# Kernel tuning notes

Measured on AMD Instinct MI355X. Metric: run time of the kernel, lower is better.

## Reference

```python
import jax, jax.numpy as jnp
import numpy as np

N, E, D, H, OUT = 100000, 1600000, 64, 64, 4


def _glorot(key, i, o):
    s = (6.0 / (i + o)) ** 0.5
    return jax.random.uniform(key, (i, o), jnp.float32, -s, s)


def setup_inputs() -> dict:
    key = jax.random.key(0)
    ks = jax.random.split(key, 5)
    x = jax.random.normal(ks[0], (N, D), jnp.float32)
    edge_index = jax.random.randint(ks[1], (2, E), 0, N, jnp.int32)
    return {
        "x": x,
        "edge_index": edge_index,
        "W0": _glorot(ks[2], D, H), "b0": jnp.zeros((H,), jnp.float32),
        "W1": _glorot(ks[3], H, H), "b1": jnp.zeros((H,), jnp.float32),
        "W2": _glorot(ks[4], H, OUT), "b2": jnp.zeros((OUT,), jnp.float32),
    }


def _gcn_layer(x, src, dst, W, b):
    # WeightedGCNConv.forward: remove_self_loops, then gcn_norm with
    # add_self_loops=True (self-loop weight 1), symmetric normalization,
    # scatter-add aggregation, then Linear.
    n = x.shape[0]
    w = (src != dst).astype(x.dtype)           # zero out original self loops
    deg = jax.ops.segment_sum(w, dst, num_segments=n) + 1.0  # +1 from added self loop
    dis = jax.lax.rsqrt(deg)                   # deg >= 1, no inf
    norm = dis[src] * w * dis[dst]             # [E]
    agg = jax.ops.segment_sum(norm[:, None] * x[src], dst, num_segments=n)
    agg = agg + (dis * dis)[:, None] * x       # self-loop contribution
    return agg @ W + b


def reference(x, edge_index, W0, b0, W1, b1, W2, b2):
    src, dst = edge_index[0], edge_index[1]    # flow source_to_target
    # Dropout is identity in eval mode.
    h = jax.nn.relu(_gcn_layer(x, src, dst, W0, b0))
    h = jax.nn.relu(_gcn_layer(h, src, dst, W1, b1))
    return _gcn_layer(h, src, dst, W2, b2)     # [N, 4]
```

## Files before the change

### kernel.cpp

```cpp
#include <hip/hip_runtime.h>
#include <hip/hip_fp16.h>


#define BLK 256
#define NBITS 7
#define NBW   (1 << NBITS)
#define G     8
#define CHUNK 4096
#define EPT   (CHUNK / BLK)
#define CAPG  384
#define PAD   16

__global__ void k_binA(const int* __restrict__ src, const int* __restrict__ dst,
                       int* __restrict__ bcur, int* __restrict__ binned,
                       int E, int nb) {
    __shared__ int lcnt[1024];
    __shared__ int lbase[1024];
    int t = threadIdx.x;
    int g = blockIdx.x & (G - 1);
    for (int i = t; i < nb; i += BLK) lcnt[i] = 0;
    __syncthreads();

    int e0 = blockIdx.x * CHUNK;
    int bs[EPT], vs[EPT];
#pragma unroll
    for (int i = 0; i < EPT; ++i) {
        int e = e0 + i * BLK + t;
        bs[i] = -1;
        if (e < E) {
            int s = src[e], d = dst[e];
            if (s != d) {
                bs[i] = d >> NBITS;
                vs[i] = (s << NBITS) | (d & (NBW - 1));
                atomicAdd(&lcnt[bs[i]], 1);
            }
        }
    }
    __syncthreads();
    for (int i = t; i < nb; i += BLK) {
        int c = lcnt[i];
        lbase[i] = c ? atomicAdd(&bcur[(g * nb + i) * PAD], c) : 0;
    }
    __syncthreads();
    for (int i = t; i < nb; i += BLK) lcnt[i] = 0;
    __syncthreads();
#pragma unroll
    for (int i = 0; i < EPT; ++i) {
        if (bs[i] >= 0) {
            int p = lbase[bs[i]] + atomicAdd(&lcnt[bs[i]], 1);
            if (p < CAPG) binned[(size_t)(g * nb + bs[i]) * CAPG + p] = vs[i];
        }
    }
}

__global__ void k_bscan(const int* __restrict__ bcur, int* __restrict__ bbase, int nb) {
    __shared__ int sh[1024];
    int t = threadIdx.x;
    int v = 0;
    if (t < nb)
        for (int g = 0; g < G; ++g) v += min(bcur[(g * nb + t) * PAD], CAPG);
    sh[t] = v;
    __syncthreads();
    for (int off = 1; off < 1024; off <<= 1) {
        int u = (t >= off) ? sh[t - off] : 0;
        __syncthreads();
        sh[t] += u;
        __syncthreads();
    }
    if (t < nb) bbase[t] = sh[t] - v;
}

__global__ void k_binB(const int* __restrict__ bcur, const int* __restrict__ binned,
                       const int* __restrict__ bbase, int* __restrict__ rowstart,
                       float* __restrict__ dis, int* __restrict__ srcs,
                       int n, int nb) {
    __shared__ int cnt[NBW];
    __shared__ int scan[NBW];
    int b = blockIdx.x;
    int t = threadIdx.x;
    if (t < NBW) cnt[t] = 0;
    __syncthreads();
    for (int g = 0; g < G; ++g) {
        int m = min(bcur[(g * nb + b) * PAD], CAPG);
        const int* reg = binned + (size_t)(g * nb + b) * CAPG;
        for (int i = t; i < m; i += BLK)
            atomicAdd(&cnt[reg[i] & (NBW - 1)], 1);
    }
    __syncthreads();
    int c = 0;
    if (t < NBW) { c = cnt[t]; scan[t] = c; }
    __syncthreads();
    for (int off = 1; off < NBW; off <<= 1) {
        int u = (t < NBW && t >= off) ? scan[t - off] : 0;
        __syncthreads();
        if (t < NBW) scan[t] += u;
        __syncthreads();
    }
    int base = bbase[b];
    if (t < NBW) {
        int excl = scan[t] - c;
        int node = b * NBW + t;
        if (node < n) {
            rowstart[node] = base + excl;
            dis[node] = rsqrtf((float)c + 1.0f);
        }
        if (node == n) rowstart[n] = base + excl;
    }
    __syncthreads();
    if (t < NBW) scan[t] = scan[t] - c;
    __syncthreads();
    for (int g = 0; g < G; ++g) {
        int m = min(bcur[(g * nb + b) * PAD], CAPG);
        const int* reg = binned + (size_t)(g * nb + b) * CAPG;
        for (int i = t; i < m; i += BLK) {
            int v = reg[i];
            int p = atomicAdd(&scan[v & (NBW - 1)], 1);
            srcs[base + p] = v >> NBITS;
        }
    }
}

__global__ void k_gemm64(const float* __restrict__ in, const float* __restrict__ W,
                         const float* __restrict__ dis, __half* __restrict__ z16, int n) {
    __shared__ float rows[4][64];
    int c  = threadIdx.x & 63;
    int r4 = threadIdx.x >> 6;
    float Wr[64];
#pragma unroll
    for (int k = 0; k < 64; ++k) Wr[k] = W[k * 64 + c];
    const float4* rp = reinterpret_cast<const float4*>(&rows[r4][0]);
    for (long base = (long)blockIdx.x * 4; base < n; base += (long)gridDim.x * 4) {
        long row = base + r4;
        __syncthreads();
        if (row < n) rows[r4][c] = in[row * 64 + c];
        __syncthreads();
        if (row < n) {
            float acc = 0.0f;
#pragma unroll
            for (int k4 = 0; k4 < 16; ++k4) {
                float4 rv = rp[k4];
                acc = fmaf(rv.x, Wr[4 * k4 + 0], acc);
                acc = fmaf(rv.y, Wr[4 * k4 + 1], acc);
                acc = fmaf(rv.z, Wr[4 * k4 + 2], acc);
                acc = fmaf(rv.w, Wr[4 * k4 + 3], acc);
            }
            z16[row * 64 + c] = __float2half(dis[row] * acc);
        }
    }
}

__device__ __forceinline__ float4 gather_row(const float2* __restrict__ zrow,
                                             const int* __restrict__ rowstart,
                                             const int* __restrict__ srcs,
                                             int node, int lane, int p, int hi) {
    float4 acc = make_float4(0.f, 0.f, 0.f, 0.f);
    if (hi == 0) {
        float2 r = zrow[(long)node * 16 + p];
        float2 a = __half22float2(*reinterpret_cast<__half2*>(&r.x));
        float2 bq = __half22float2(*reinterpret_cast<__half2*>(&r.y));
        acc = make_float4(a.x, a.y, bq.x, bq.y);
    }
    int beg = rowstart[node], end = rowstart[node + 1];
    for (int base = beg; base < end; base += 64) {
        int m = min(end - base, 64);
        int s = (lane < m) ? srcs[base + lane] : 0;
        int mf = m & ~3;
#pragma unroll 8
        for (int j = 0; j < mf; j += 4) {
            int sj = __shfl(s, j + hi);
            float2 r = zrow[(long)sj * 16 + p];
            float2 a = __half22float2(*reinterpret_cast<__half2*>(&r.x));
            float2 bq = __half22float2(*reinterpret_cast<__half2*>(&r.y));
            acc.x += a.x; acc.y += a.y; acc.z += bq.x; acc.w += bq.y;
        }
        if (m & 3) {
            int idx = mf + hi;
            int sj = __shfl(s, idx < 64 ? idx : 63);
            if (idx < m) {
                float2 r = zrow[(long)sj * 16 + p];
                float2 a = __half22float2(*reinterpret_cast<__half2*>(&r.x));
                float2 bq = __half22float2(*reinterpret_cast<__half2*>(&r.y));
                acc.x += a.x; acc.y += a.y; acc.z += bq.x; acc.w += bq.y;
            }
        }
    }
    acc.x += __shfl_xor(acc.x, 16); acc.y += __shfl_xor(acc.y, 16);
    acc.z += __shfl_xor(acc.z, 16); acc.w += __shfl_xor(acc.w, 16);
    acc.x += __shfl_xor(acc.x, 32); acc.y += __shfl_xor(acc.y, 32);
    acc.z += __shfl_xor(acc.z, 32); acc.w += __shfl_xor(acc.w, 32);
    return acc;
}

__global__ void k_aggW1(const float2* __restrict__ zrow, const int* __restrict__ rowstart,
                        const int* __restrict__ srcs, const float* __restrict__ dis,
                        const float* __restrict__ b0, const float* __restrict__ W1,
                        __half* __restrict__ z1, int n) {
    __shared__ float hrow[4][64];
    int lane = threadIdx.x & 63;
    int wv   = threadIdx.x >> 6;
    int node = blockIdx.x * (BLK / 64) + wv;
    if (node >= n) return;
    int p = lane & 15, hi = lane >> 4;

    float4 acc = gather_row(zrow, rowstart, srcs, node, lane, p, hi);

    float dd = dis[node];
    float4 bb = reinterpret_cast<const float4*>(b0)[p];
    if (hi == 0) {
        float4 h;
        h.x = fmaxf(dd * acc.x + bb.x, 0.f);
        h.y = fmaxf(dd * acc.y + bb.y, 0.f);
        h.z = fmaxf(dd * acc.z + bb.z, 0.f);
        h.w = fmaxf(dd * acc.w + bb.w, 0.f);
        *reinterpret_cast<float4*>(&hrow[wv][4 * p]) = h;
    }
    asm volatile("s_waitcnt lgkmcnt(0)" ::: "memory");

    float Wr[64];
#pragma unroll
    for (int k = 0; k < 64; ++k) Wr[k] = W1[k * 64 + lane];
    const float4* hq = reinterpret_cast<const float4*>(&hrow[wv][0]);
    float o = 0.f;
#pragma unroll
    for (int k4 = 0; k4 < 16; ++k4) {
        float4 hv = hq[k4];
        o = fmaf(hv.x, Wr[4 * k4 + 0], o);
        o = fmaf(hv.y, Wr[4 * k4 + 1], o);
        o = fmaf(hv.z, Wr[4 * k4 + 2], o);
        o = fmaf(hv.w, Wr[4 * k4 + 3], o);
    }
    z1[(long)node * 64 + lane] = __float2half(dd * o);
}

__global__ void k_aggW2(const float2* __restrict__ zrow, const int* __restrict__ rowstart,
                        const int* __restrict__ srcs, const float* __restrict__ dis,
                        const float* __restrict__ b1, const float* __restrict__ W2,
                        float* __restrict__ y2, int n) {
    __shared__ float W2l[64 * 4];
    if (threadIdx.x < 256) W2l[threadIdx.x] = W2[threadIdx.x];
    __syncthreads();
    int lane = threadIdx.x & 63;
    int node = blockIdx.x * (BLK / 64) + (threadIdx.x >> 6);
    if (node >= n) return;
    int p = lane & 15, hi = lane >> 4;

    float4 acc = gather_row(zrow, rowstart, srcs, node, lane, p, hi);

    float dd = dis[node];
    float4 bb = reinterpret_cast<const float4*>(b1)[p];
    float h0 = fmaxf(dd * acc.x + bb.x, 0.f);
    float h1 = fmaxf(dd * acc.y + bb.y, 0.f);
    float h2 = fmaxf(dd * acc.z + bb.z, 0.f);
    float h3 = fmaxf(dd * acc.w + bb.w, 0.f);
    float pc[4];
#pragma unroll
    for (int c = 0; c < 4; ++c) {
        pc[c] = h0 * W2l[(4 * p + 0) * 4 + c] + h1 * W2l[(4 * p + 1) * 4 + c]
              + h2 * W2l[(4 * p + 2) * 4 + c] + h3 * W2l[(4 * p + 3) * 4 + c];
    }
#pragma unroll
    for (int off = 1; off < 16; off <<= 1) {
#pragma unroll
        for (int c = 0; c < 4; ++c) pc[c] += __shfl_xor(pc[c], off);
    }
    if (lane == 0) {
        reinterpret_cast<float4*>(y2)[node] =
            make_float4(dd * pc[0], dd * pc[1], dd * pc[2], dd * pc[3]);
    }
}

__global__ void k_agg4(const float* __restrict__ z2, const int* __restrict__ rowstart,
                       const int* __restrict__ srcs, const float* __restrict__ dis,
                       const float* __restrict__ b, float* __restrict__ out, int n) {
    long t = (long)blockIdx.x * blockDim.x + threadIdx.x;
    int i = (int)(t >> 2), c = (int)(t & 3);
    if (i < n) {
        float acc = z2[(long)i * 4 + c];
        int beg = rowstart[i], end = rowstart[i + 1];
        for (int e = beg; e < end; ++e)
            acc += z2[(long)srcs[e] * 4 + c];
        out[(long)i * 4 + c] = dis[i] * acc + b[c];
    }
}

extern "C" void kernel_launch(void* const* d_in, const int* in_sizes, int n_in,
                              void* d_out, int out_size, void* d_ws, size_t ws_size,
                              hipStream_t stream) {
    const float* x  = (const float*)d_in[0];
    const int*   ei = (const int*)d_in[1];
    const float* W0 = (const float*)d_in[2];
    const float* b0 = (const float*)d_in[3];
    const float* W1 = (const float*)d_in[4];
    const float* b1 = (const float*)d_in[5];
    const float* W2 = (const float*)d_in[6];
    const float* b2 = (const float*)d_in[7];
    float* out = (float*)d_out;

    const int n = in_sizes[0] / 64;
    const int E = in_sizes[1] / 2;
    const int* src = ei;
    const int* dst = ei + E;
    const int nb = (n + NBW - 1) / NBW;

    int*    bcur     = (int*)d_ws;
    int*    bbase    = bcur + G * nb * PAD;
    int*    rowstart = bbase + nb + 1;
    int*    srcs     = rowstart + n + 1;
    float*  dis      = (float*)(srcs + E);
    __half* z16      = (__half*)(dis + n);
    __half* z1       = z16 + (size_t)n * 64;
    float*  y2       = (float*)(z1 + (size_t)n * 64);
    int*    binned   = (int*)z1;

    const int gWave  = (n + (BLK / 64) - 1) / (BLK / 64);
    const int gN4    = (int)(((long)n * 4 + BLK - 1) / BLK);
    const int gGemm  = 2048;
    const int nchunk = (E + CHUNK - 1) / CHUNK;

    hipMemsetAsync(bcur, 0, (size_t)G * nb * PAD * sizeof(int), stream);
    k_binA<<<nchunk, BLK, 0, stream>>>(src, dst, bcur, binned, E, nb);
    k_bscan<<<1, 1024, 0, stream>>>(bcur, bbase, nb);
    k_binB<<<nb, BLK, 0, stream>>>(bcur, binned, bbase, rowstart, dis, srcs, n, nb);

    k_gemm64<<<gGemm, BLK, 0, stream>>>(x, W0, dis, z16, n);

    k_aggW1<<<gWave, BLK, 0, stream>>>((const float2*)z16, rowstart, srcs, dis, b0, W1,
                                       z1, n);

    k_aggW2<<<gWave, BLK, 0, stream>>>((const float2*)z1, rowstart, srcs, dis, b1, W2,
                                       y2, n);

    k_agg4<<<gN4, BLK, 0, stream>>>(y2, rowstart, srcs, dis, b2, out, n);
}
```

Baseline: 252.2 us.

## Replace bin scan kernel with atomic cursor and stage W1 as half2 in LDS

The single-block bucket prefix scan kernel is removed. Each binB block now reserves its output range with an atomicAdd on a global cursor, and rows are described by (start, count) pairs instead of a CSR rowstart array. This removes one serial launch, at the cost of a non-deterministic CSR order across buckets. Separately, aggW1 stages W1 in shared memory as transposed half2 instead of loading 64 weights per lane into registers. That cuts register pressure and global weight reloads, but it introduces fp16 rounding of the weights.

```diff
diff --git a/kernel.cpp b/kernel.cpp
--- a/kernel.cpp
+++ b/kernel.cpp
@@ -53,29 +53,13 @@
     }
 }
 
-__global__ void k_bscan(const int* __restrict__ bcur, int* __restrict__ bbase, int nb) {
-    __shared__ int sh[1024];
-    int t = threadIdx.x;
-    int v = 0;
-    if (t < nb)
-        for (int g = 0; g < G; ++g) v += min(bcur[(g * nb + t) * PAD], CAPG);
-    sh[t] = v;
-    __syncthreads();
-    for (int off = 1; off < 1024; off <<= 1) {
-        int u = (t >= off) ? sh[t - off] : 0;
-        __syncthreads();
-        sh[t] += u;
-        __syncthreads();
-    }
-    if (t < nb) bbase[t] = sh[t] - v;
-}
-
 __global__ void k_binB(const int* __restrict__ bcur, const int* __restrict__ binned,
-                       const int* __restrict__ bbase, int* __restrict__ rowstart,
+                       int* __restrict__ cursor, int2* __restrict__ rowinfo,
                        float* __restrict__ dis, int* __restrict__ srcs,
                        int n, int nb) {
     __shared__ int cnt[NBW];
     __shared__ int scan[NBW];
+    __shared__ int sbase;
     int b = blockIdx.x;
     int t = threadIdx.x;
     if (t < NBW) cnt[t] = 0;
@@ -96,15 +80,16 @@
         if (t < NBW) scan[t] += u;
         __syncthreads();
     }
-    int base = bbase[b];
+    if (t == NBW - 1) sbase = atomicAdd(cursor, scan[NBW - 1]);
+    __syncthreads();
+    int base = sbase;
     if (t < NBW) {
         int excl = scan[t] - c;
         int node = b * NBW + t;
         if (node < n) {
-            rowstart[node] = base + excl;
+            rowinfo[node] = make_int2(base + excl, c);
             dis[node] = rsqrtf((float)c + 1.0f);
         }
-        if (node == n) rowstart[n] = base + excl;
     }
     __syncthreads();
     if (t < NBW) scan[t] = scan[t] - c;
@@ -150,7 +135,7 @@
 }
 
 __device__ __forceinline__ float4 gather_row(const float2* __restrict__ zrow,
-                                             const int* __restrict__ rowstart,
+                                             const int2* __restrict__ rowinfo,
                                              const int* __restrict__ srcs,
                                              int node, int lane, int p, int hi) {
     float4 acc = make_float4(0.f, 0.f, 0.f, 0.f);
@@ -160,7 +145,8 @@
         float2 bq = __half22float2(*reinterpret_cast<__half2*>(&r.y));
         acc = make_float4(a.x, a.y, bq.x, bq.y);
     }
-    int beg = rowstart[node], end = rowstart[node + 1];
+    int2 ri = rowinfo[node];
+    int beg = ri.x, end = ri.x + ri.y;
     for (int base = beg; base < end; base += 64) {
         int m = min(end - base, 64);
         int s = (lane < m) ? srcs[base + lane] : 0;
@@ -191,18 +177,25 @@
     return acc;
 }
 
-__global__ void k_aggW1(const float2* __restrict__ zrow, const int* __restrict__ rowstart,
+__global__ void k_aggW1(const float2* __restrict__ zrow, const int2* __restrict__ rowinfo,
                         const int* __restrict__ srcs, const float* __restrict__ dis,
                         const float* __restrict__ b0, const float* __restrict__ W1,
                         __half* __restrict__ z1, int n) {
+    __shared__ __half2 W1t[32 * 64];
     __shared__ float hrow[4][64];
+    for (int i = threadIdx.x; i < 32 * 64; i += BLK) {
+        int c = i & 63, k2 = i >> 6;
+        W1t[i] = __floats2half2_rn(W1[(2 * k2) * 64 + c], W1[(2 * k2 + 1) * 64 + c]);
+    }
+    __syncthreads();
+
     int lane = threadIdx.x & 63;
     int wv   = threadIdx.x >> 6;
     int node = blockIdx.x * (BLK / 64) + wv;
     if (node >= n) return;
     int p = lane & 15, hi = lane >> 4;
 
-    float4 acc = gather_row(zrow, rowstart, srcs, node, lane, p, hi);
+    float4 acc = gather_row(zrow, rowinfo, srcs, node, lane, p, hi);
 
     float dd = dis[node];
     float4 bb = reinterpret_cast<const float4*>(b0)[p];
@@ -216,23 +209,22 @@
     }
     asm volatile("s_waitcnt lgkmcnt(0)" ::: "memory");
 
-    float Wr[64];
-#pragma unroll
-    for (int k = 0; k < 64; ++k) Wr[k] = W1[k * 64 + lane];
     const float4* hq = reinterpret_cast<const float4*>(&hrow[wv][0]);
     float o = 0.f;
 #pragma unroll
     for (int k4 = 0; k4 < 16; ++k4) {
         float4 hv = hq[k4];
-        o = fmaf(hv.x, Wr[4 * k4 + 0], o);
-        o = fmaf(hv.y, Wr[4 * k4 + 1], o);
-        o = fmaf(hv.z, Wr[4 * k4 + 2], o);
-        o = fmaf(hv.w, Wr[4 * k4 + 3], o);
+        float2 wa = __half22float2(W1t[(2 * k4 + 0) * 64 + lane]);
+        float2 wb = __half22float2(W1t[(2 * k4 + 1) * 64 + lane]);
+        o = fmaf(hv.x, wa.x, o);
+        o = fmaf(hv.y, wa.y, o);
+        o = fmaf(hv.z, wb.x, o);
+        o = fmaf(hv.w, wb.y, o);
     }
     z1[(long)node * 64 + lane] = __float2half(dd * o);
 }
 
-__global__ void k_aggW2(const float2* __restrict__ zrow, const int* __restrict__ rowstart,
+__global__ void k_aggW2(const float2* __restrict__ zrow, const int2* __restrict__ rowinfo,
                         const int* __restrict__ srcs, const float* __restrict__ dis,
                         const float* __restrict__ b1, const float* __restrict__ W2,
                         float* __restrict__ y2, int n) {
@@ -244,7 +236,7 @@
     if (node >= n) return;
     int p = lane & 15, hi = lane >> 4;
 
-    float4 acc = gather_row(zrow, rowstart, srcs, node, lane, p, hi);
+    float4 acc = gather_row(zrow, rowinfo, srcs, node, lane, p, hi);
 
     float dd = dis[node];
     float4 bb = reinterpret_cast<const float4*>(b1)[p];
@@ -269,14 +261,15 @@
     }
 }
 
-__global__ void k_agg4(const float* __restrict__ z2, const int* __restrict__ rowstart,
+__global__ void k_agg4(const float* __restrict__ z2, const int2* __restrict__ rowinfo,
                        const int* __restrict__ srcs, const float* __restrict__ dis,
                        const float* __restrict__ b, float* __restrict__ out, int n) {
     long t = (long)blockIdx.x * blockDim.x + threadIdx.x;
     int i = (int)(t >> 2), c = (int)(t & 3);
     if (i < n) {
         float acc = z2[(long)i * 4 + c];
-        int beg = rowstart[i], end = rowstart[i + 1];
+        int2 ri = rowinfo[i];
+        int beg = ri.x, end = ri.x + ri.y;
         for (int e = beg; e < end; ++e)
             acc += z2[(long)srcs[e] * 4 + c];
         out[(long)i * 4 + c] = dis[i] * acc + b[c];
@@ -303,9 +296,9 @@
     const int nb = (n + NBW - 1) / NBW;
 
     int*    bcur     = (int*)d_ws;
-    int*    bbase    = bcur + G * nb * PAD;
-    int*    rowstart = bbase + nb + 1;
-    int*    srcs     = rowstart + n + 1;
+    int*    cursor   = bcur + G * nb * PAD;
+    int2*   rowinfo  = (int2*)(cursor + 16);
+    int*    srcs     = (int*)(rowinfo + n);
     float*  dis      = (float*)(srcs + E);
     __half* z16      = (__half*)(dis + n);
     __half* z1       = z16 + (size_t)n * 64;
@@ -317,18 +310,17 @@
     const int gGemm  = 2048;
     const int nchunk = (E + CHUNK - 1) / CHUNK;
 
-    hipMemsetAsync(bcur, 0, (size_t)G * nb * PAD * sizeof(int), stream);
+    hipMemsetAsync(bcur, 0, ((size_t)G * nb * PAD + 16) * sizeof(int), stream);
     k_binA<<<nchunk, BLK, 0, stream>>>(src, dst, bcur, binned, E, nb);
-    k_bscan<<<1, 1024, 0, stream>>>(bcur, bbase, nb);
-    k_binB<<<nb, BLK, 0, stream>>>(bcur, binned, bbase, rowstart, dis, srcs, n, nb);
+    k_binB<<<nb, BLK, 0, stream>>>(bcur, binned, cursor, rowinfo, dis, srcs, n, nb);
 
     k_gemm64<<<gGemm, BLK, 0, stream>>>(x, W0, dis, z16, n);
 
-    k_aggW1<<<gWave, BLK, 0, stream>>>((const float2*)z16, rowstart, srcs, dis, b0, W1,
+    k_aggW1<<<gWave, BLK, 0, stream>>>((const float2*)z16, rowinfo, srcs, dis, b0, W1,
                                        z1, n);
 
-    k_aggW2<<<gWave, BLK, 0, stream>>>((const float2*)z1, rowstart, srcs, dis, b1, W2,
+    k_aggW2<<<gWave, BLK, 0, stream>>>((const float2*)z1, rowinfo, srcs, dis, b1, W2,
                                        y2, n);
 
-    k_agg4<<<gN4, BLK, 0, stream>>>(y2, rowstart, srcs, dis, b2, out, n);
-}
+    k_agg4<<<gN4, BLK, 0, stream>>>(y2, rowinfo, srcs, dis, b2, out, n);
+}
```

Measured after the change: 248.3 us. About the same (-1.5%).
